# Kernel tuning notes

Measured on AMD Instinct MI355X. Metric: run time of the kernel, lower is better.

Reference implementation:

```python
import jax, jax.numpy as jnp
import numpy as np

AUX_COEF = 0.001
Z_COEF = 0.001


def setup_inputs() -> dict:
    key = jax.random.key(0)
    ks = jax.random.split(key, 6)
    B, S, H, E, F = 4, 2048, 1024, 8, 2048
    scale_h = 1.0 / np.sqrt(H)
    scale_f = 1.0 / np.sqrt(F)
    return {
        "hidden_states": jax.random.normal(ks[0], (B, S, H), jnp.float32),
        "router_w": jax.random.normal(ks[1], (E, H), jnp.float32) * scale_h,
        "w1": jax.random.normal(ks[2], (E, H, F), jnp.float32) * scale_h,
        "b1": jax.random.normal(ks[3], (E, F), jnp.float32) * 0.01,
        "w2": jax.random.normal(ks[4], (E, F, H), jnp.float32) * scale_f,
        "b2": jax.random.normal(ks[5], (E, H), jnp.float32) * 0.01,
        "num_experts_per_tok": 2,
    }


def reference(hidden_states, router_w, w1, b1, w2, b2, num_experts_per_tok):
    B, S, H = hidden_states.shape
    E = router_w.shape[0]
    x = hidden_states.reshape(-1, H)  # [T, H]

    # Router
    logits = jnp.einsum('th,eh->te', x, router_w)  # [T, E]
    logp = jax.nn.log_softmax(logits, axis=-1)
    probs = jnp.exp(logp)

    # Top-k routing mask (note: original code does NOT weight by top_k probs)
    _, top_idx = jax.lax.top_k(probs, num_experts_per_tok)  # [T, K]
    mask = jax.nn.one_hot(top_idx, E, dtype=x.dtype).sum(axis=-2)  # [T, E] 0/1

    # Losses: KL(probs || uniform) with torch kl_div(batchmean over dim0=B) + z-loss
    ideal = 1.0 / E
    aux_loss = (ideal * (jnp.log(jnp.float32(ideal)) - logp)).sum() / B * AUX_COEF
    z_loss = jnp.mean(jnp.square(logits)) * Z_COEF
    router_loss = aux_loss + z_loss

    # Dense grouped expert MLP, combined with 0/1 routing mask
    h = jnp.einsum('th,ehf->tef', x, w1) + b1  # [T, E, F]
    h = jax.nn.silu(h)
    y = jnp.einsum('tef,efh->teh', h, w2) + b2  # [T, E, H]
    out = jnp.einsum('teh,te->th', y, mask).reshape(B, S, H)
    return out, router_loss
```

## Files before the change

kernel.cpp:

```cpp
#include <hip/hip_runtime.h>
#include <stdint.h>

#define T_TOK 8192
#define H_DIM 1024
#define E_NUM 8
#define F_DIM 2048
#define BATCH 4
#define AUX_COEF 0.001f
#define Z_COEF 0.001f

#define BM 128
#define BN 128
#define BK 64

#define NBLK_TOK 32
#define CAP_TILES 32

typedef __bf16 bf16x8 __attribute__((ext_vector_type(8)));
typedef float f32x4 __attribute__((ext_vector_type(4)));

__device__ __forceinline__ unsigned short f2bf(float f) {
    union { float f; uint32_t u; } v; v.f = f;
    uint32_t u = v.u;
    return (unsigned short)((u + 0x7FFFu + ((u >> 16) & 1u)) >> 16);
}
__device__ __forceinline__ float bf2f(unsigned short u) {
    union { uint32_t u; float f; } v; v.u = ((uint32_t)u) << 16; return v.f;
}

__device__ __forceinline__ void gl_lds16(const void* g, void* l) {
    __builtin_amdgcn_global_load_lds((const __attribute__((address_space(1))) uint32_t*)g,
                                     (__attribute__((address_space(3))) uint32_t*)l, 16, 0, 0);
}

__global__ void transpose_conv_kernel(const float* __restrict__ in, unsigned short* __restrict__ out,
                                      int R, int C) {
    __shared__ float tile[32][33];
    int e = blockIdx.z;
    const float* ine = in + (size_t)e * R * C;
    unsigned short* oute = out + (size_t)e * R * C;
    int tx = threadIdx.x & 31, ty = threadIdx.x >> 5;
    int c0 = blockIdx.x * 32, r0 = blockIdx.y * 32;
#pragma unroll
    for (int i = 0; i < 4; i++) {
        int r = r0 + ty + i * 8;
        tile[ty + i * 8][tx] = ine[(size_t)r * C + c0 + tx];
    }
    __syncthreads();
#pragma unroll
    for (int i = 0; i < 4; i++) {
        int c = c0 + ty + i * 8;
        oute[(size_t)c * R + r0 + tx] = f2bf(tile[tx][ty + i * 8]);
    }
}

__global__ void router_kernel(const float* __restrict__ x, const float* __restrict__ rw,
                              unsigned short* __restrict__ xb,
                              int* __restrict__ top2, float2* __restrict__ loss_part) {
    int wave = threadIdx.x >> 6;
    int lane = threadIdx.x & 63;
    int t = blockIdx.x * 4 + wave;
    const float4* xr = (const float4*)(x + (size_t)t * H_DIM);
    float4 xv[4];
#pragma unroll
    for (int k = 0; k < 4; k++) xv[k] = xr[lane + 64 * k];
    uint2* xo = (uint2*)(xb + (size_t)t * H_DIM);
#pragma unroll
    for (int k = 0; k < 4; k++) {
        uint2 o;
        o.x = (uint32_t)f2bf(xv[k].x) | ((uint32_t)f2bf(xv[k].y) << 16);
        o.y = (uint32_t)f2bf(xv[k].z) | ((uint32_t)f2bf(xv[k].w) << 16);
        xo[lane + 64 * k] = o;
    }
    float acc[E_NUM];
#pragma unroll
    for (int e = 0; e < E_NUM; e++) {
        const float4* rr = (const float4*)(rw + e * H_DIM);
        float s = 0.f;
#pragma unroll
        for (int k = 0; k < 4; k++) {
            float4 r = rr[lane + 64 * k];
            s += xv[k].x * r.x + xv[k].y * r.y + xv[k].z * r.z + xv[k].w * r.w;
        }
        acc[e] = s;
    }
#pragma unroll
    for (int e = 0; e < E_NUM; e++) {
        float v = acc[e];
#pragma unroll
        for (int off = 32; off; off >>= 1) v += __shfl_xor(v, off);
        acc[e] = v;
    }
    __shared__ float red[8];
    if (lane == 0) {
        float mx = acc[0];
#pragma unroll
        for (int e = 1; e < E_NUM; e++) mx = fmaxf(mx, acc[e]);
        float s = 0.f;
#pragma unroll
        for (int e = 0; e < E_NUM; e++) s += expf(acc[e] - mx);
        float lse = mx + logf(s);
        float slogp = 0.f, ssq = 0.f;
#pragma unroll
        for (int e = 0; e < E_NUM; e++) { slogp += acc[e] - lse; ssq += acc[e] * acc[e]; }
        int i1 = 0; float m1 = acc[0];
#pragma unroll
        for (int e = 1; e < E_NUM; e++) if (acc[e] > m1) { m1 = acc[e]; i1 = e; }
        int i2 = -1; float m2 = -1e30f;
#pragma unroll
        for (int e = 0; e < E_NUM; e++) if (e != i1 && acc[e] > m2) { m2 = acc[e]; i2 = e; }
        top2[t] = i1 | (i2 << 8);
        red[wave] = slogp;
        red[4 + wave] = ssq;
    }
    __syncthreads();
    if (threadIdx.x == 0) {
        float2 p;
        p.x = red[0] + red[1] + red[2] + red[3];
        p.y = red[4] + red[5] + red[6] + red[7];
        loss_part[blockIdx.x] = p;
    }
}

__global__ void hist_kernel(const int* __restrict__ top2, int* __restrict__ blockcounts) {
    __shared__ int cnt[E_NUM];
    if (threadIdx.x < E_NUM) cnt[threadIdx.x] = 0;
    __syncthreads();
    int t = blockIdx.x * 256 + threadIdx.x;
    int v = top2[t];
    atomicAdd(&cnt[v & 255], 1);
    atomicAdd(&cnt[v >> 8], 1);
    __syncthreads();
    if (threadIdx.x < E_NUM) blockcounts[blockIdx.x * E_NUM + threadIdx.x] = cnt[threadIdx.x];
}

__global__ void scan_kernel(const int* __restrict__ blockcounts, const float2* __restrict__ loss_part,
                            int* __restrict__ counts, int* __restrict__ basep, int* __restrict__ offs,
                            float* __restrict__ loss_out) {
    __shared__ float redx[4], redy[4];
    int tid = threadIdx.x;
    float sx = 0.f, sy = 0.f;
    for (int i = tid; i < T_TOK / 4; i += 256) {
        float2 p = loss_part[i];
        sx += p.x; sy += p.y;
    }
#pragma unroll
    for (int off = 32; off; off >>= 1) { sx += __shfl_xor(sx, off); sy += __shfl_xor(sy, off); }
    if ((tid & 63) == 0) { redx[tid >> 6] = sx; redy[tid >> 6] = sy; }
    __syncthreads();
    if (tid == 0) {
        float slogp = redx[0] + redx[1] + redx[2] + redx[3];
        float ssq = redy[0] + redy[1] + redy[2] + redy[3];
        float ideal = 1.0f / E_NUM;
        float aux = ideal * ((float)T_TOK * E_NUM * logf(ideal) - slogp) / BATCH * AUX_COEF;
        float z = ssq / ((float)T_TOK * E_NUM) * Z_COEF;
        loss_out[0] = aux + z;
    }
    if (tid < E_NUM) {
        int s = 0;
        for (int b = 0; b < NBLK_TOK; b++) s += blockcounts[b * E_NUM + tid];
        counts[tid] = s;
    }
    __syncthreads();
    if (tid == 0) {
        int s = 0;
        for (int e = 0; e < E_NUM; e++) { basep[e] = s; s += counts[e]; }
    }
    __syncthreads();
    if (tid < E_NUM) {
        int o = basep[tid];
        for (int b = 0; b < NBLK_TOK; b++) { offs[b * E_NUM + tid] = o; o += blockcounts[b * E_NUM + tid]; }
    }
}

__global__ void scatter_kernel(const int* __restrict__ top2, const int* __restrict__ offs,
                               int* __restrict__ rowlist, int* __restrict__ posv) {
    __shared__ int cur[E_NUM];
    if (threadIdx.x < E_NUM) cur[threadIdx.x] = 0;
    __syncthreads();
    int t = blockIdx.x * 256 + threadIdx.x;
    int v = top2[t];
    int e0 = v & 255, e1 = v >> 8;
    int r0 = atomicAdd(&cur[e0], 1);
    int r1 = atomicAdd(&cur[e1], 1);
    int p0 = offs[blockIdx.x * E_NUM + e0] + r0;
    int p1 = offs[blockIdx.x * E_NUM + e1] + r1;
    rowlist[p0] = t;
    rowlist[p1] = t;
    posv[t] = p0 | (p1 << 16);
}

__global__ void combine_kernel(const int* __restrict__ top2, const int* __restrict__ posv,
                               const unsigned short* __restrict__ ybuf, const float* __restrict__ b2,
                               float* __restrict__ out) {
    int t = blockIdx.x;
    int v = top2[t];
    int p = posv[t];
    int e0 = v & 255, e1 = v >> 8;
    int p0 = p & 0xffff, p1 = (p >> 16) & 0xffff;
    int i = threadIdx.x;
    const ushort4* y0 = (const ushort4*)(ybuf + (size_t)p0 * H_DIM);
    const ushort4* y1 = (const ushort4*)(ybuf + (size_t)p1 * H_DIM);
    const float4* q0 = (const float4*)(b2 + (size_t)e0 * H_DIM);
    const float4* q1 = (const float4*)(b2 + (size_t)e1 * H_DIM);
    ushort4 a = y0[i], b = y1[i];
    float4 c0 = q0[i], c1 = q1[i];
    float4 o;
    o.x = bf2f(a.x) + bf2f(b.x) + c0.x + c1.x;
    o.y = bf2f(a.y) + bf2f(b.y) + c0.y + c1.y;
    o.z = bf2f(a.z) + bf2f(b.z) + c0.z + c1.z;
    o.w = bf2f(a.w) + bf2f(b.w) + c0.w + c1.w;
    ((float4*)(out + (size_t)t * H_DIM))[i] = o;
}


__global__ __launch_bounds__(256)
void gemm1_kernel(const unsigned short* __restrict__ xb,
                  const unsigned short* __restrict__ w1t,
                  const float* __restrict__ b1,
                  const int* __restrict__ rowlist, const int* __restrict__ basep,
                  const int* __restrict__ counts,
                  unsigned short* __restrict__ h1)
{
    int bid = blockIdx.x;
    int e = bid & 7;
    int q = bid >> 3;
    int nt = q & 15;
    int mt = q >> 4;
    int n_e = counts[e];
    if (mt * BM >= n_e) return;
    int base_e = basep[e];

    __shared__ __attribute__((aligned(16))) unsigned short ldsA[BM * BK];
    __shared__ __attribute__((aligned(16))) unsigned short ldsB[BN * BK];

    int tid = threadIdx.x;
    int srow = tid >> 3;
    int schunk = (tid & 7) ^ (srow & 7);
    const unsigned short* aP[4];
    const unsigned short* bP[4];
#pragma unroll
    for (int ro = 0; ro < 4; ro++) {
        int r = srow + 32 * ro;
        int ra = min(mt * BM + r, n_e - 1);
        int tok = rowlist[base_e + ra];
        aP[ro] = xb + (size_t)tok * H_DIM + schunk * 8;
        bP[ro] = w1t + ((size_t)e * F_DIM + nt * BN + r) * H_DIM + schunk * 8;
    }

    int wv = tid >> 6, lane = tid & 63;
    int wm = (wv & 1) * 64, wn = (wv >> 1) * 64;
    int mlane = lane & 15, quad = lane >> 4;
    int qa = quad << 4;

    char* lA = (char*)ldsA + wv * 1024;
    char* lB = (char*)ldsB + wv * 1024;

    f32x4 acc[4][4] = {};

    int abase[4], axor[4], bbase[4], bxor[4];
#pragma unroll
    for (int i = 0; i < 4; i++) {
        int ra = wm + i * 16 + mlane;
        abase[i] = ra * 128; axor[i] = (ra & 7) << 4;
        int rb = wn + i * 16 + mlane;
        bbase[i] = rb * 128; bxor[i] = (rb & 7) << 4;
    }

    for (int k0 = 0; k0 < H_DIM; k0 += BK) {
        __syncthreads();
#pragma unroll
        for (int ro = 0; ro < 4; ro++) {
            gl_lds16(aP[ro] + k0, lA + ro * 4096);
            gl_lds16(bP[ro] + k0, lB + ro * 4096);
        }
        __syncthreads();
#pragma unroll
        for (int ks = 0; ks < 2; ks++) {
            int koff = ks * 64 + qa;
            bf16x8 af[4], bfr[4];
#pragma unroll
            for (int i = 0; i < 4; i++) {
                af[i] = *(const bf16x8*)((char*)ldsA + abase[i] + (koff ^ axor[i]));
                bfr[i] = *(const bf16x8*)((char*)ldsB + bbase[i] + (koff ^ bxor[i]));
            }
#pragma unroll
            for (int mi = 0; mi < 4; mi++)
#pragma unroll
                for (int ni = 0; ni < 4; ni++)
                    acc[mi][ni] = __builtin_amdgcn_mfma_f32_16x16x32_bf16(af[mi], bfr[ni], acc[mi][ni], 0, 0, 0);
        }
    }

#pragma unroll
    for (int mi = 0; mi < 4; mi++) {
        int mbase = mt * BM + wm + mi * 16 + quad * 4;
#pragma unroll
        for (int ni = 0; ni < 4; ni++) {
            int gf = nt * BN + wn + ni * 16 + mlane;
            float bias = b1[e * F_DIM + gf];
#pragma unroll
            for (int r = 0; r < 4; r++) {
                int m = mbase + r;
                if (m < n_e) {
                    float c = acc[mi][ni][r] + bias;
                    float sv = c / (1.f + __expf(-c));
                    h1[(size_t)(base_e + m) * F_DIM + gf] = f2bf(sv);
                }
            }
        }
    }
}

__global__ __launch_bounds__(256)
void gemm2_kernel(const unsigned short* __restrict__ h1,
                  const unsigned short* __restrict__ w2t,
                  const int* __restrict__ basep,
                  const int* __restrict__ counts,
                  unsigned short* __restrict__ ybuf)
{
    int bid = blockIdx.x;
    int e = bid & 7;
    int q = bid >> 3;
    int nt = q & 7;
    int mt = q >> 3;
    int n_e = counts[e];
    if (mt * BM >= n_e) return;
    int base_e = basep[e];

    __shared__ __attribute__((aligned(16))) unsigned short ldsA[BM * BK];
    __shared__ __attribute__((aligned(16))) unsigned short ldsB[BN * BK];

    int tid = threadIdx.x;
    int srow = tid >> 3;
    int schunk = (tid & 7) ^ (srow & 7);
    const unsigned short* aP[4];
    const unsigned short* bP[4];
#pragma unroll
    for (int ro = 0; ro < 4; ro++) {
        int r = srow + 32 * ro;
        int ra = base_e + min(mt * BM + r, n_e - 1);
        aP[ro] = h1 + (size_t)ra * F_DIM + schunk * 8;
        bP[ro] = w2t + ((size_t)e * H_DIM + nt * BN + r) * F_DIM + schunk * 8;
    }

    int wv = tid >> 6, lane = tid & 63;
    int wm = (wv & 1) * 64, wn = (wv >> 1) * 64;
    int mlane = lane & 15, quad = lane >> 4;
    int qa = quad << 4;

    char* lA = (char*)ldsA + wv * 1024;
    char* lB = (char*)ldsB + wv * 1024;

    f32x4 acc[4][4] = {};

    int abase[4], axor[4], bbase[4], bxor[4];
#pragma unroll
    for (int i = 0; i < 4; i++) {
        int ra = wm + i * 16 + mlane;
        abase[i] = ra * 128; axor[i] = (ra & 7) << 4;
        int rb = wn + i * 16 + mlane;
        bbase[i] = rb * 128; bxor[i] = (rb & 7) << 4;
    }

    for (int k0 = 0; k0 < F_DIM; k0 += BK) {
        __syncthreads();
#pragma unroll
        for (int ro = 0; ro < 4; ro++) {
            gl_lds16(aP[ro] + k0, lA + ro * 4096);
            gl_lds16(bP[ro] + k0, lB + ro * 4096);
        }
        __syncthreads();
#pragma unroll
        for (int ks = 0; ks < 2; ks++) {
            int koff = ks * 64 + qa;
            bf16x8 af[4], bfr[4];
#pragma unroll
            for (int i = 0; i < 4; i++) {
                af[i] = *(const bf16x8*)((char*)ldsA + abase[i] + (koff ^ axor[i]));
                bfr[i] = *(const bf16x8*)((char*)ldsB + bbase[i] + (koff ^ bxor[i]));
            }
#pragma unroll
            for (int mi = 0; mi < 4; mi++)
#pragma unroll
                for (int ni = 0; ni < 4; ni++)
                    acc[mi][ni] = __builtin_amdgcn_mfma_f32_16x16x32_bf16(af[mi], bfr[ni], acc[mi][ni], 0, 0, 0);
        }
    }

#pragma unroll
    for (int mi = 0; mi < 4; mi++) {
        int mbase = mt * BM + wm + mi * 16 + quad * 4;
#pragma unroll
        for (int r = 0; r < 4; r++) {
            int m = mbase + r;
            if (m < n_e) {
                unsigned short* yr = ybuf + (size_t)(base_e + m) * H_DIM + nt * BN + wn + mlane;
#pragma unroll
                for (int ni = 0; ni < 4; ni++)
                    yr[ni * 16] = f2bf(acc[mi][ni][r]);
            }
        }
    }
}

extern "C" void kernel_launch(void* const* d_in, const int* in_sizes, int n_in,
                              void* d_out, int out_size, void* d_ws, size_t ws_size,
                              hipStream_t stream) {
    const float* x = (const float*)d_in[0];
    const float* rw = (const float*)d_in[1];
    const float* w1 = (const float*)d_in[2];
    const float* b1 = (const float*)d_in[3];
    const float* w2 = (const float*)d_in[4];
    const float* b2 = (const float*)d_in[5];
    float* out = (float*)d_out;

    char* ws = (char*)d_ws;
    int* counts      = (int*)(ws + 0);
    int* basep       = (int*)(ws + 64);
    int* blockcounts = (int*)(ws + 128);
    int* offs        = (int*)(ws + 2048);
    float2* loss_part = (float2*)(ws + 4096);
    int* top2        = (int*)(ws + 32768);
    int* rowlist     = (int*)(ws + 65536);
    int* posv        = (int*)(ws + 131072);
    unsigned short* xb  = (unsigned short*)(ws + 163840);
    unsigned short* w1t = (unsigned short*)(ws + 163840 + 16777216ULL);
    unsigned short* w2t = (unsigned short*)(ws + 163840 + 16777216ULL + 33554432ULL);
    unsigned short* h1  = (unsigned short*)(ws + 163840 + 16777216ULL + 2ULL * 33554432ULL);
    unsigned short* ybuf = w1t;

    transpose_conv_kernel<<<dim3(64, 32, 8), 256, 0, stream>>>(w1, w1t, H_DIM, F_DIM);
    transpose_conv_kernel<<<dim3(32, 64, 8), 256, 0, stream>>>(w2, w2t, F_DIM, H_DIM);
    router_kernel<<<T_TOK / 4, 256, 0, stream>>>(x, rw, xb, top2, loss_part);
    hist_kernel<<<NBLK_TOK, 256, 0, stream>>>(top2, blockcounts);
    scan_kernel<<<1, 256, 0, stream>>>(blockcounts, loss_part, counts, basep, offs,
                                       out + (size_t)T_TOK * H_DIM);
    scatter_kernel<<<NBLK_TOK, 256, 0, stream>>>(top2, offs, rowlist, posv);
    gemm1_kernel<<<8 * CAP_TILES * (F_DIM / BN), 256, 0, stream>>>(xb, w1t, b1, rowlist, basep, counts, h1);
    gemm2_kernel<<<8 * CAP_TILES * (H_DIM / BN), 256, 0, stream>>>(h1, w2t, basep, counts, ybuf);
    combine_kernel<<<T_TOK, 256, 0, stream>>>(top2, posv, ybuf, b2, out);
}
```

Baseline: 452.9 us.

## Replace grouped expert GEMMs with 256x256-tile kernel using 4-stage LDS ring

Merges the two per-expert GEMM kernels into one templated kernel. It uses 256x256 output tiles with 512 threads and a BK=32 K-step. Global-to-LDS async loads go into a 4-deep ring buffer, with explicit vmcnt waits, a single barrier per K-step, and raised wave priority around the MFMA blocks, so loads stay three tiles ahead of compute. The aims are higher arithmetic intensity per block and hiding load latency that the old two-barrier, single-buffer loop exposed. Costs: the XOR swizzle is dropped, which may cause LDS bank conflicts. The 128KB of LDS per block limits occupancy to one block per CU. Larger tiles also waste more work on partially filled expert tiles.

```diff
diff --git a/kernel.cpp b/kernel.cpp
--- a/kernel.cpp
+++ b/kernel.cpp
@@ -9,12 +9,12 @@
 #define AUX_COEF 0.001f
 #define Z_COEF 0.001f
 
-#define BM 128
-#define BN 128
-#define BK 64
-
 #define NBLK_TOK 32
-#define CAP_TILES 32
+
+#define GBM 256
+#define GBN 256
+#define GBK 32
+#define MT_CAP 16
 
 typedef __bf16 bf16x8 __attribute__((ext_vector_type(8)));
 typedef float f32x4 __attribute__((ext_vector_type(4)));
@@ -213,192 +213,133 @@
     ((float4*)(out + (size_t)t * H_DIM))[i] = o;
 }
 
-
-__global__ __launch_bounds__(256)
-void gemm1_kernel(const unsigned short* __restrict__ xb,
-                  const unsigned short* __restrict__ w1t,
-                  const float* __restrict__ b1,
-                  const int* __restrict__ rowlist, const int* __restrict__ basep,
-                  const int* __restrict__ counts,
-                  unsigned short* __restrict__ h1)
+template<int KD, int NTILES_N, bool IS_G1>
+__global__ __launch_bounds__(512, 2)
+void gemm_big(const unsigned short* __restrict__ A,
+              const unsigned short* __restrict__ Bt,
+              const float* __restrict__ bias_p,
+              const int* __restrict__ rowlist,
+              const int* __restrict__ basep,
+              const int* __restrict__ counts,
+              unsigned short* __restrict__ Out)
 {
+    constexpr int ND = NTILES_N * GBN;
+    constexpr int NKT = KD / GBK;
+    static_assert(NKT >= 4, "ring needs >=4 K-tiles");
+
     int bid = blockIdx.x;
     int e = bid & 7;
     int q = bid >> 3;
-    int nt = q & 15;
-    int mt = q >> 4;
+    int nt = q % NTILES_N;
+    int mt = q / NTILES_N;
     int n_e = counts[e];
-    if (mt * BM >= n_e) return;
+    if (mt * GBM >= n_e) return;
     int base_e = basep[e];
 
-    __shared__ __attribute__((aligned(16))) unsigned short ldsA[BM * BK];
-    __shared__ __attribute__((aligned(16))) unsigned short ldsB[BN * BK];
+    __shared__ __attribute__((aligned(16))) unsigned char lds[4 * 32768];
 
     int tid = threadIdx.x;
-    int srow = tid >> 3;
-    int schunk = (tid & 7) ^ (srow & 7);
-    const unsigned short* aP[4];
-    const unsigned short* bP[4];
-#pragma unroll
-    for (int ro = 0; ro < 4; ro++) {
-        int r = srow + 32 * ro;
-        int ra = min(mt * BM + r, n_e - 1);
-        int tok = rowlist[base_e + ra];
-        aP[ro] = xb + (size_t)tok * H_DIM + schunk * 8;
-        bP[ro] = w1t + ((size_t)e * F_DIM + nt * BN + r) * H_DIM + schunk * 8;
-    }
-
     int wv = tid >> 6, lane = tid & 63;
-    int wm = (wv & 1) * 64, wn = (wv >> 1) * 64;
+
+    int srow = tid >> 2;
+    int schunk = tid & 3;
+    const unsigned short* aS[2];
+    const unsigned short* bS[2];
+#pragma unroll
+    for (int c = 0; c < 2; c++) {
+        int r = c * 128 + srow;
+        if (IS_G1) {
+            int ra = min(mt * GBM + r, n_e - 1);
+            int tok = rowlist[base_e + ra];
+            aS[c] = A + (size_t)tok * KD + schunk * 8;
+        } else {
+            int ra = base_e + min(mt * GBM + r, n_e - 1);
+            aS[c] = A + (size_t)ra * KD + schunk * 8;
+        }
+        bS[c] = Bt + ((size_t)e * ND + nt * GBN + r) * KD + schunk * 8;
+    }
+    char* ldsw = (char*)lds + wv * 1024;
+
     int mlane = lane & 15, quad = lane >> 4;
-    int qa = quad << 4;
-
-    char* lA = (char*)ldsA + wv * 1024;
-    char* lB = (char*)ldsB + wv * 1024;
-
-    f32x4 acc[4][4] = {};
-
-    int abase[4], axor[4], bbase[4], bxor[4];
-#pragma unroll
-    for (int i = 0; i < 4; i++) {
-        int ra = wm + i * 16 + mlane;
-        abase[i] = ra * 128; axor[i] = (ra & 7) << 4;
-        int rb = wn + i * 16 + mlane;
-        bbase[i] = rb * 128; bxor[i] = (rb & 7) << 4;
-    }
-
-    for (int k0 = 0; k0 < H_DIM; k0 += BK) {
-        __syncthreads();
-#pragma unroll
-        for (int ro = 0; ro < 4; ro++) {
-            gl_lds16(aP[ro] + k0, lA + ro * 4096);
-            gl_lds16(bP[ro] + k0, lB + ro * 4096);
+    int wr = (wv >> 2) * 128;
+    int wc = (wv & 3) * 64;
+    int aOff[8], bOff[4];
+#pragma unroll
+    for (int mi = 0; mi < 8; mi++) aOff[mi] = (wr + mi * 16 + mlane) * 64 + quad * 16;
+#pragma unroll
+    for (int ni = 0; ni < 4; ni++) bOff[ni] = 16384 + (wc + ni * 16 + mlane) * 64 + quad * 16;
+
+    f32x4 acc[8][4] = {};
+
+    auto stage = [&](int t) {
+        char* sb = ldsw + (size_t)(t & 3) * 32768;
+        const unsigned short* a0 = aS[0] + t * GBK;
+        const unsigned short* a1 = aS[1] + t * GBK;
+        const unsigned short* b0 = bS[0] + t * GBK;
+        const unsigned short* b1 = bS[1] + t * GBK;
+        gl_lds16(a0, sb);
+        gl_lds16(a1, sb + 8192);
+        gl_lds16(b0, sb + 16384);
+        gl_lds16(b1, sb + 24576);
+    };
+    auto compute = [&](int t) {
+        char* sb = (char*)lds + (size_t)(t & 3) * 32768;
+        __builtin_amdgcn_s_setprio(1);
+        bf16x8 bfr[4];
+#pragma unroll
+        for (int ni = 0; ni < 4; ni++) bfr[ni] = *(const bf16x8*)(sb + bOff[ni]);
+#pragma unroll
+        for (int mi = 0; mi < 8; mi++) {
+            bf16x8 af = *(const bf16x8*)(sb + aOff[mi]);
+#pragma unroll
+            for (int ni = 0; ni < 4; ni++)
+                acc[mi][ni] = __builtin_amdgcn_mfma_f32_16x16x32_bf16(af, bfr[ni], acc[mi][ni], 0, 0, 0);
         }
-        __syncthreads();
-#pragma unroll
-        for (int ks = 0; ks < 2; ks++) {
-            int koff = ks * 64 + qa;
-            bf16x8 af[4], bfr[4];
-#pragma unroll
-            for (int i = 0; i < 4; i++) {
-                af[i] = *(const bf16x8*)((char*)ldsA + abase[i] + (koff ^ axor[i]));
-                bfr[i] = *(const bf16x8*)((char*)ldsB + bbase[i] + (koff ^ bxor[i]));
-            }
-#pragma unroll
-            for (int mi = 0; mi < 4; mi++)
-#pragma unroll
-                for (int ni = 0; ni < 4; ni++)
-                    acc[mi][ni] = __builtin_amdgcn_mfma_f32_16x16x32_bf16(af[mi], bfr[ni], acc[mi][ni], 0, 0, 0);
-        }
-    }
-
-#pragma unroll
-    for (int mi = 0; mi < 4; mi++) {
-        int mbase = mt * BM + wm + mi * 16 + quad * 4;
-#pragma unroll
-        for (int ni = 0; ni < 4; ni++) {
-            int gf = nt * BN + wn + ni * 16 + mlane;
-            float bias = b1[e * F_DIM + gf];
-#pragma unroll
-            for (int r = 0; r < 4; r++) {
-                int m = mbase + r;
-                if (m < n_e) {
-                    float c = acc[mi][ni][r] + bias;
-                    float sv = c / (1.f + __expf(-c));
-                    h1[(size_t)(base_e + m) * F_DIM + gf] = f2bf(sv);
-                }
-            }
-        }
-    }
-}
-
-__global__ __launch_bounds__(256)
-void gemm2_kernel(const unsigned short* __restrict__ h1,
-                  const unsigned short* __restrict__ w2t,
-                  const int* __restrict__ basep,
-                  const int* __restrict__ counts,
-                  unsigned short* __restrict__ ybuf)
-{
-    int bid = blockIdx.x;
-    int e = bid & 7;
-    int q = bid >> 3;
-    int nt = q & 7;
-    int mt = q >> 3;
-    int n_e = counts[e];
-    if (mt * BM >= n_e) return;
-    int base_e = basep[e];
-
-    __shared__ __attribute__((aligned(16))) unsigned short ldsA[BM * BK];
-    __shared__ __attribute__((aligned(16))) unsigned short ldsB[BN * BK];
-
-    int tid = threadIdx.x;
-    int srow = tid >> 3;
-    int schunk = (tid & 7) ^ (srow & 7);
-    const unsigned short* aP[4];
-    const unsigned short* bP[4];
-#pragma unroll
-    for (int ro = 0; ro < 4; ro++) {
-        int r = srow + 32 * ro;
-        int ra = base_e + min(mt * BM + r, n_e - 1);
-        aP[ro] = h1 + (size_t)ra * F_DIM + schunk * 8;
-        bP[ro] = w2t + ((size_t)e * H_DIM + nt * BN + r) * F_DIM + schunk * 8;
-    }
-
-    int wv = tid >> 6, lane = tid & 63;
-    int wm = (wv & 1) * 64, wn = (wv >> 1) * 64;
-    int mlane = lane & 15, quad = lane >> 4;
-    int qa = quad << 4;
-
-    char* lA = (char*)ldsA + wv * 1024;
-    char* lB = (char*)ldsB + wv * 1024;
-
-    f32x4 acc[4][4] = {};
-
-    int abase[4], axor[4], bbase[4], bxor[4];
-#pragma unroll
-    for (int i = 0; i < 4; i++) {
-        int ra = wm + i * 16 + mlane;
-        abase[i] = ra * 128; axor[i] = (ra & 7) << 4;
-        int rb = wn + i * 16 + mlane;
-        bbase[i] = rb * 128; bxor[i] = (rb & 7) << 4;
-    }
-
-    for (int k0 = 0; k0 < F_DIM; k0 += BK) {
-        __syncthreads();
-#pragma unroll
-        for (int ro = 0; ro < 4; ro++) {
-            gl_lds16(aP[ro] + k0, lA + ro * 4096);
-            gl_lds16(bP[ro] + k0, lB + ro * 4096);
-        }
-        __syncthreads();
-#pragma unroll
-        for (int ks = 0; ks < 2; ks++) {
-            int koff = ks * 64 + qa;
-            bf16x8 af[4], bfr[4];
-#pragma unroll
-            for (int i = 0; i < 4; i++) {
-                af[i] = *(const bf16x8*)((char*)ldsA + abase[i] + (koff ^ axor[i]));
-                bfr[i] = *(const bf16x8*)((char*)ldsB + bbase[i] + (koff ^ bxor[i]));
-            }
-#pragma unroll
-            for (int mi = 0; mi < 4; mi++)
-#pragma unroll
-                for (int ni = 0; ni < 4; ni++)
-                    acc[mi][ni] = __builtin_amdgcn_mfma_f32_16x16x32_bf16(af[mi], bfr[ni], acc[mi][ni], 0, 0, 0);
-        }
-    }
-
-#pragma unroll
-    for (int mi = 0; mi < 4; mi++) {
-        int mbase = mt * BM + wm + mi * 16 + quad * 4;
+        __builtin_amdgcn_s_setprio(0);
+    };
+
+    stage(0); stage(1); stage(2);
+
+    for (int kt = 0; kt < NKT - 3; ++kt) {
+        asm volatile("s_waitcnt vmcnt(8) lgkmcnt(0)" ::: "memory");
+        __builtin_amdgcn_s_barrier();
+        __builtin_amdgcn_sched_barrier(0);
+        stage(kt + 3);
+        compute(kt);
+    }
+    asm volatile("s_waitcnt vmcnt(8) lgkmcnt(0)" ::: "memory");
+    __builtin_amdgcn_s_barrier();
+    __builtin_amdgcn_sched_barrier(0);
+    compute(NKT - 3);
+    asm volatile("s_waitcnt vmcnt(4) lgkmcnt(0)" ::: "memory");
+    __builtin_amdgcn_s_barrier();
+    __builtin_amdgcn_sched_barrier(0);
+    compute(NKT - 2);
+    asm volatile("s_waitcnt vmcnt(0) lgkmcnt(0)" ::: "memory");
+    __builtin_amdgcn_s_barrier();
+    __builtin_amdgcn_sched_barrier(0);
+    compute(NKT - 1);
+
+    float bias[4];
+#pragma unroll
+    for (int ni = 0; ni < 4; ni++) {
+        if (IS_G1) bias[ni] = bias_p[(size_t)e * ND + nt * GBN + wc + ni * 16 + mlane];
+        else bias[ni] = 0.f;
+    }
+#pragma unroll
+    for (int mi = 0; mi < 8; mi++) {
+        int mbase = mt * GBM + wr + mi * 16 + quad * 4;
 #pragma unroll
         for (int r = 0; r < 4; r++) {
             int m = mbase + r;
             if (m < n_e) {
-                unsigned short* yr = ybuf + (size_t)(base_e + m) * H_DIM + nt * BN + wn + mlane;
-#pragma unroll
-                for (int ni = 0; ni < 4; ni++)
-                    yr[ni * 16] = f2bf(acc[mi][ni][r]);
+                unsigned short* orow = Out + (size_t)(base_e + m) * ND + nt * GBN + wc + mlane;
+#pragma unroll
+                for (int ni = 0; ni < 4; ni++) {
+                    float c = acc[mi][ni][r] + bias[ni];
+                    if (IS_G1) c = c / (1.f + __expf(-c));
+                    orow[ni * 16] = f2bf(c);
+                }
             }
         }
     }
@@ -437,7 +378,9 @@
     scan_kernel<<<1, 256, 0, stream>>>(blockcounts, loss_part, counts, basep, offs,
                                        out + (size_t)T_TOK * H_DIM);
     scatter_kernel<<<NBLK_TOK, 256, 0, stream>>>(top2, offs, rowlist, posv);
-    gemm1_kernel<<<8 * CAP_TILES * (F_DIM / BN), 256, 0, stream>>>(xb, w1t, b1, rowlist, basep, counts, h1);
-    gemm2_kernel<<<8 * CAP_TILES * (H_DIM / BN), 256, 0, stream>>>(h1, w2t, basep, counts, ybuf);
+    gemm_big<H_DIM, F_DIM / GBN, true><<<8 * MT_CAP * (F_DIM / GBN), 512, 0, stream>>>(
+        xb, w1t, b1, rowlist, basep, counts, h1);
+    gemm_big<F_DIM, H_DIM / GBN, false><<<8 * MT_CAP * (H_DIM / GBN), 512, 0, stream>>>(
+        h1, w2t, nullptr, rowlist, basep, counts, ybuf);
     combine_kernel<<<T_TOK, 256, 0, stream>>>(top2, posv, ybuf, b2, out);
 }
```

Result: no change. 453.6 us (+0.2%).
